# Performance work log

Hardware: AMD Instinct MI355X
Metric: run time of the kernel (lower is better)

The kernel has to match this reference:

```python
import jax, jax.numpy as jnp
import numpy as np

B, S, E, H, T, V = 32, 512, 256, 512, 8, 32000
G = 4 * H  # gate width


def setup_inputs() -> dict:
    key = jax.random.key(0)
    ks = jax.random.split(key, 14)
    s = 0.02  # init scale to keep tanh/sigmoid out of saturation
    return {
        "x": jax.random.randint(ks[0], (B, S), 0, V),
        "TASK": 0,
        "embed": jax.random.normal(ks[1], (V, E), jnp.float32) * s,
        "Wx_t": jax.random.normal(ks[2], (T, E, G), jnp.float32) * s,
        "Wh_t": jax.random.normal(ks[3], (T, H, G), jnp.float32) * s,
        "b_t": jnp.zeros((T, G), jnp.float32),
        "Ws_p1": jax.random.normal(ks[4], (H, H), jnp.float32) * s,
        "Ws_p2": jax.random.normal(ks[5], (H + E, H), jnp.float32) * s,
        "Us_w": jax.random.normal(ks[6], (H, 1), jnp.float32) * s,
        "Us_b": jnp.zeros((1,), jnp.float32),
        "Wx_c": jax.random.normal(ks[7], (E, G), jnp.float32) * s,
        "Wh_c": jax.random.normal(ks[8], (H, G), jnp.float32) * s,
        "Wm_c": jax.random.normal(ks[9], (H, G), jnp.float32) * s,
        "b_c": jnp.zeros((G,), jnp.float32),
    }


def _lstm_cell(g, c):
    i, f, gg, o = jnp.split(g, 4, axis=-1)
    c_new = jax.nn.sigmoid(f) * c + jax.nn.sigmoid(i) * jnp.tanh(gg)
    h_new = jax.nn.sigmoid(o) * jnp.tanh(c_new)
    return h_new, c_new


def _task_messages(emb, Wx, Wh, b):
    # emb [B,S,E]; Wx [K,E,4H]; returns aggregated messages [S,B,H,K]
    K = Wx.shape[0]
    xg = jnp.einsum('bse,keg->skbg', emb, Wx)  # precompute input gates [S,K,B,4H]
    h0 = jnp.zeros((K, emb.shape[0], Wh.shape[1]), emb.dtype)

    def step(carry, xg_t):
        h, c = carry  # [K,B,H]
        g = xg_t + jnp.einsum('kbh,khg->kbg', h, Wh) + b[:, None, :]
        h, c = _lstm_cell(g, c)
        return (h, c), h

    _, hs = jax.lax.scan(step, (h0, h0), xg)  # hs [S,K,B,H]
    return jnp.transpose(hs, (0, 2, 3, 1))  # [S,B,H,K]


def reference(x, TASK, embed, Wx_t, Wh_t, b_t, Ws_p1, Ws_p2, Us_w, Us_b,
              Wx_c, Wh_c, Wm_c, b_c):
    emb = embed[x]  # [B,S,E]
    other = np.array([i for i in range(Wx_t.shape[0]) if i != TASK])
    agg = _task_messages(emb, Wx_t[other], Wh_t[other], b_t[other])  # [S,B,H,K]

    emb_s = jnp.swapaxes(emb, 0, 1)          # [S,B,E]
    xg_c = emb_s @ Wx_c                       # [S,B,4H] precomputed input gates
    Bsz, Hdim = x.shape[0], Wh_c.shape[0]
    h0 = jnp.zeros((Bsz, Hdim), emb.dtype)

    def step(carry, inp):
        h, c = carry
        agg_t, emb_t, xg_t = inp  # [B,H,K], [B,E], [B,4H]
        # attention over the K task messages
        v1 = jnp.einsum('ij,bjk->bik', Ws_p1, agg_t) \
             + (jnp.concatenate([h, emb_t], axis=-1) @ Ws_p2)[:, :, None]
        v2 = jnp.tanh(v1)                                  # [B,H,K]
        Si = jnp.einsum('bhk,ho->bk', v2, Us_w) + Us_b     # [B,K]
        a = jax.nn.softmax(Si, axis=1)
        Rt = jnp.einsum('bk,bhk->bh', a, agg_t)            # [B,H]
        # custom LSTM cell step with message input Rt
        g = xg_t + h @ Wh_c + Rt @ Wm_c + b_c
        h, c = _lstm_cell(g, c)
        return (h, c), h

    (hN, cN), outs = jax.lax.scan(step, (h0, h0), (agg, emb_s, xg_c))
    out = jnp.swapaxes(outs, 0, 1)  # [B,S,H]
    return out, hN
```

## Files before the change

kernel.cpp:

```cpp
#include <hip/hip_runtime.h>

#define S_ 512
#define SCOPE __HIP_MEMORY_SCOPE_AGENT

typedef short bf16x8 __attribute__((ext_vector_type(8)));
typedef float f32x4 __attribute__((ext_vector_type(4)));

__device__ __forceinline__ float sigm(float x) { return 1.f / (1.f + expf(-x)); }
__device__ __forceinline__ float b2f(unsigned short u) {
    return __builtin_bit_cast(float, (unsigned)u << 16);
}
__device__ __forceinline__ unsigned short f2b(float f) {
    unsigned x = __builtin_bit_cast(unsigned, f);
    return (unsigned short)((x + 0x7fffu + ((x >> 16) & 1u)) >> 16);
}
__device__ __forceinline__ float ldcf(const float* p) {
    return __hip_atomic_load(p, __ATOMIC_RELAXED, SCOPE);
}
__device__ __forceinline__ unsigned ldc32(const void* p) {
    return __hip_atomic_load((const unsigned*)p, __ATOMIC_RELAXED, SCOPE);
}
__device__ __forceinline__ unsigned long long ldc64(const void* p) {
    return __hip_atomic_load((const unsigned long long*)p, __ATOMIC_RELAXED, SCOPE);
}
__device__ __forceinline__ void stg32(void* p, unsigned v) {
    __hip_atomic_store((unsigned*)p, v, __ATOMIC_RELAXED, SCOPE);
}
__device__ __forceinline__ void stgf(float* p, float v) {
    __hip_atomic_store(p, v, __ATOMIC_RELAXED, SCOPE);
}
__device__ __forceinline__ bf16x8 frag_c(const unsigned short* p) {
    union { unsigned long long q[2]; bf16x8 v; } u;
    u.q[0] = ldc64(p); u.q[1] = ldc64(p + 4);
    return u.v;
}
__device__ __forceinline__ bf16x8 frag_p(const unsigned short* p) {
    return *(const bf16x8*)p;
}
__device__ __forceinline__ void spin_ge(unsigned* p, unsigned thr) {
    while (__hip_atomic_load(p, __ATOMIC_RELAXED, SCOPE) < thr)
        __builtin_amdgcn_s_sleep(1);
}

__device__ __forceinline__ void gbar(unsigned* bar, int tid, int wg, unsigned n) {
    __syncthreads();
    if (tid == 0) {
        int g = wg >> 5;
        unsigned* gcnt = bar + 64 + g * 32;
        unsigned* ggen = bar + 320 + g * 32;
        unsigned old = __hip_atomic_fetch_add(gcnt, 1u, __ATOMIC_RELAXED, SCOPE);
        if (old == n * 32u - 1u) {
            unsigned rold = __hip_atomic_fetch_add(bar, 1u, __ATOMIC_RELAXED, SCOPE);
            if (rold == n * 8u - 1u) {
                __hip_atomic_store(bar + 32, n, __ATOMIC_RELAXED, SCOPE);
            } else {
                while (__hip_atomic_load(bar + 32, __ATOMIC_RELAXED, SCOPE) < n)
                    __builtin_amdgcn_s_sleep(1);
            }
            __hip_atomic_store(ggen, n, __ATOMIC_RELAXED, SCOPE);
        } else {
            while (__hip_atomic_load(ggen, __ATOMIC_RELAXED, SCOPE) < n)
                __builtin_amdgcn_s_sleep(1);
        }
        asm volatile("" ::: "memory");
    }
    __syncthreads();
}

__device__ __forceinline__ void gbar2(unsigned* bar, int tid, int wg, unsigned bn) {
    __syncthreads();
    if (tid == 0) stg32(bar + 1024 + wg * 32, bn);
    if (wg == 0) {
        if (tid < 256) spin_ge(bar + 1024 + tid * 32, bn);
        __syncthreads();
        if (tid == 0) stg32(bar + 576, bn);
    } else {
        if (tid == 0) spin_ge(bar + 576, bn);
        __syncthreads();
    }
}

__global__ __launch_bounds__(512) void fused_all(
        const int* __restrict__ x, const int* __restrict__ taskp,
        const float* __restrict__ embed,
        const float* __restrict__ Wx_t, const float* __restrict__ Wh_t,
        const float* __restrict__ b_t,
        const float* __restrict__ Ws_p1, const float* __restrict__ Ws_p2,
        const float* __restrict__ Us_w,
        const float* __restrict__ Wx_c, const float* __restrict__ Wh_c,
        const float* __restrict__ Wm_c, const float* __restrict__ b_c,
        float* __restrict__ out,
        unsigned short* __restrict__ WTa,  unsigned short* __restrict__ WTp2,
        unsigned short* __restrict__ WTp1, unsigned short* __restrict__ WTc,
        unsigned short* __restrict__ embbf, unsigned short* __restrict__ hbf,
        unsigned short* __restrict__ hmbf,
        float* __restrict__ ctask, float* __restrict__ cmain,
        float* __restrict__ p2w, float* __restrict__ partial,
        float* __restrict__ hNf, unsigned* __restrict__ bar)
{
    __shared__ float smem[8320];
    __shared__ unsigned short swA[64 * 776];
    const int wg = blockIdx.x, tid = threadIdx.x;
    const int lane = tid & 63, wave = tid >> 6;
    const int rowm = lane & 15, ks = lane >> 4;
    const int task = taskp[0];
    unsigned bn = 0;

    for (int i = wg * 512 + tid; i < 114688; i += 131072) stg32((unsigned*)hbf + i, 0u);
    for (int i = wg * 512 + tid; i < 16384; i += 131072) stg32((unsigned*)hmbf + i, 0u);
    for (int i = wg * 512 + tid; i < 114688; i += 131072) stgf(ctask + i, 0.f);
    for (int i = wg * 512 + tid; i < 16384; i += 131072) stgf(cmain + i, 0.f);
    for (int i = wg * 512 + tid; i < 2097152; i += 131072) {
        int ts = i >> 12, b = (i >> 7) & 31, ep = i & 127;
        int tok = x[b * S_ + ts];
        const float* s = embed + (size_t)tok * 256 + 2 * ep;
        stg32((unsigned*)embbf + i, (unsigned)f2b(s[0]) | ((unsigned)f2b(s[1]) << 16));
    }
    for (int i = wg * 512 + tid; i < 5505024; i += 131072) {
        int s = i / 24576, r = i % 24576, kp = r >> 6, cg = r & 63;
        int k = s >> 5, nt = s & 31, kk = k + (k >= task);
        int col = ((cg >> 4) << 9) + nt * 16 + (cg & 15);
        int kr = kp * 2;
        const float* src = (kr < 256)
            ? Wx_t + (size_t)kk * 524288 + (size_t)kr * 2048 + col
            : Wh_t + (size_t)kk * 1048576 + (size_t)(kr - 256) * 2048 + col;
        stg32((unsigned*)WTa + (size_t)s * 24576 + cg * 384 + kp,
              (unsigned)f2b(src[0]) | ((unsigned)f2b(src[2048]) << 16));
    }
    for (int i = wg * 512 + tid; i < 196608; i += 131072) {
        int p = i / 24576, r = i % 24576, kp = r >> 6, cg = r & 63;
        int col = p * 64 + cg, kr = kp * 2;
        const float* src = Ws_p2 + (size_t)kr * 512 + col;
        stg32((unsigned*)WTp2 + p * 24576 + cg * 384 + kp,
              (unsigned)f2b(src[0]) | ((unsigned)f2b(src[512]) << 16));
    }
    for (int i = wg * 512 + tid; i < 131072; i += 131072) {
        const float* src = Ws_p1 + 2 * (size_t)i;
        stg32((unsigned*)WTp1 + i, (unsigned)f2b(src[0]) | ((unsigned)f2b(src[1]) << 16));
    }
    for (int i = wg * 512 + tid; i < 1310720; i += 131072) {
        int ntc = i / 10240, r = i % 10240, kp = r >> 4, cg = r & 15;
        int col = ((cg >> 2) << 9) + ntc * 4 + (cg & 3);
        int kr = kp * 2;
        const float* src = (kr < 256) ? Wx_c + (size_t)kr * 2048 + col
                         : (kr < 768) ? Wh_c + (size_t)(kr - 256) * 2048 + col
                                      : Wm_c + (size_t)(kr - 768) * 2048 + col;
        stg32((unsigned*)WTc + ntc * 10240 + cg * 640 + kp,
              (unsigned)f2b(src[0]) | ((unsigned)f2b(src[2048]) << 16));
    }
    gbar(bar, tid, wg, 1);

    if (wg < 232) {
        const unsigned* srcw = (const unsigned*)(wg < 224
            ? WTa + (size_t)wg * 49152 : WTp2 + (size_t)(wg - 224) * 49152);
        for (int i = tid; i < 24576; i += 512) {
            int cg = i / 384, kp = i % 384;
            ((unsigned*)(swA + cg * 776))[kp] = srcw[cg * 384 + kp];
        }
    }
    __syncthreads();

    const int xq = wg & 7, jq = wg >> 3;
    const int kB = jq >> 2, itB = xq + 8 * (jq & 3);

    for (int t = 0; t < S_; ++t) {
        const int old = t & 1, nw = old ^ 1;
        const unsigned short* hb_old = hbf + old * 114688;
        unsigned short* hb_new = hbf + nw * 114688;
        const unsigned short* hm_old = hmbf + old * 16384;
        unsigned short* hm_new = hmbf + nw * 16384;
        const unsigned short* et = embbf + (size_t)t * 8192;

        if (wg < 232) {
            const bool istask = wg < 224;
            unsigned short* sh = (unsigned short*)smem;
            const unsigned short* hsrc = istask ? hb_old + (wg >> 5) * 16384 : hm_old;
            for (int i = tid; i < 4096; i += 512) {
                int row = i >> 7, c8 = i & 127;
                *(unsigned long long*)(sh + row * 520 + c8 * 4) =
                    ldc64(hsrc + row * 512 + c8 * 4);
            }
            __syncthreads();
            f32x4 acc = {0.f, 0.f, 0.f, 0.f};
            if (istask) {
                int k = wg >> 5, nt = wg & 31;
                int mt = wave >> 2, g = wave & 3;
                int b = mt * 16 + rowm;
                const unsigned short* wtp = swA + (g * 16 + rowm) * 776;
                const unsigned short* ep_ = et + b * 256;
                const unsigned short* shb = sh + b * 520;
#pragma unroll
                for (int kt = 0; kt < 24; ++kt) {
                    int ko = kt * 32 + ks * 8;
                    bf16x8 bf = frag_p(wtp + ko);
                    bf16x8 af = (kt < 8) ? frag_p(ep_ + ko) : frag_p(shb + ko - 256);
                    acc = __builtin_amdgcn_mfma_f32_16x16x32_bf16(af, bf, acc, 0, 0, 0);
                }
                __syncthreads();
                float* sg = smem;
#pragma unroll
                for (int r2 = 0; r2 < 4; ++r2)
                    sg[(mt * 16 + (lane >> 4) * 4 + r2) * 64 + g * 16 + rowm] = acc[r2];
                __syncthreads();
                {
                    int b2 = tid >> 4, hc = tid & 15;
                    int kk = k + (k >= task);
                    const float* bb = b_t + kk * 2048 + nt * 16 + hc;
                    float gi = sg[b2 * 64 + hc]      + bb[0];
                    float gf = sg[b2 * 64 + 16 + hc] + bb[512];
                    float gg = sg[b2 * 64 + 32 + hc] + bb[1024];
                    float go = sg[b2 * 64 + 48 + hc] + bb[1536];
                    int cidx = (k * 32 + b2) * 512 + nt * 16 + hc;
                    float cold = ctask[cidx];
                    float cn = sigm(gf) * cold + sigm(gi) * tanhf(gg);
                    float hn = sigm(go) * tanhf(cn);
                    ctask[cidx] = cn;
                    int hbits = (int)f2b(hn);
                    int oth = __shfl_xor(hbits, 1, 64);
                    if ((hc & 1) == 0)
                        stg32(hb_new + cidx, (unsigned)hbits | ((unsigned)oth << 16));
                }
            } else {
                int pb = wg - 224;
                int mt = wave >> 2, q = wave & 3;
                int b = mt * 16 + rowm;
                int cg = q * 16 + rowm;
                const unsigned short* wtp = swA + cg * 776;
                const unsigned short* ep_ = et + b * 256;
                const unsigned short* shb = sh + b * 520;
#pragma unroll
                for (int kt = 0; kt < 24; ++kt) {
                    int ko = kt * 32 + ks * 8;
                    bf16x8 bf = frag_p(wtp + ko);
                    bf16x8 af = (kt < 16) ? frag_p(shb + ko) : frag_p(ep_ + ko - 512);
                    acc = __builtin_amdgcn_mfma_f32_16x16x32_bf16(af, bf, acc, 0, 0, 0);
                }
#pragma unroll
                for (int r2 = 0; r2 < 4; ++r2)
                    stgf(p2w + (mt * 16 + (lane >> 4) * 4 + r2) * 512 + pb * 64 + cg, acc[r2]);
            }
        }
        gbar2(bar, tid, wg, ++bn);

        if (wg < 224) {
            int mt = wave & 1, kq = wave >> 1;
            f32x4 acc = {0.f, 0.f, 0.f, 0.f};
            const unsigned short* wtp = WTp1 + (itB * 16 + rowm) * 512;
            const unsigned short* hp_ = hb_new + (kB * 32 + mt * 16 + rowm) * 512;
#pragma unroll
            for (int s4 = 0; s4 < 4; ++s4) {
                int ko = (kq * 4 + s4) * 32 + ks * 8;
                bf16x8 bf = frag_p(wtp + ko);
                bf16x8 af = frag_c(hp_ + ko);
                acc = __builtin_amdgcn_mfma_f32_16x16x32_bf16(af, bf, acc, 0, 0, 0);
            }
            ((f32x4*)smem)[wave * 64 + lane] = acc;
            __syncthreads();
            {
                int b2 = tid >> 4, i2 = tid & 15;
                int mt2 = b2 >> 4, rr = b2 & 15;
                int ln = ((rr & 12) << 2) | i2, rg = rr & 3;
                float val = 0.f;
#pragma unroll
                for (int q2 = 0; q2 < 4; ++q2)
                    val += smem[((q2 * 2 + mt2) * 64 + ln) * 4 + rg];
                val += ldcf(p2w + b2 * 512 + itB * 16 + i2);
                float sv = tanhf(val) * Us_w[itB * 16 + i2];
                sv += __shfl_xor(sv, 1, 64); sv += __shfl_xor(sv, 2, 64);
                sv += __shfl_xor(sv, 4, 64); sv += __shfl_xor(sv, 8, 64);
                if (i2 == 0) stgf(partial + (kB * 32 + itB) * 32 + b2, sv);
            }
        }
        gbar2(bar, tid, wg, ++bn);

        {
            int mh = wg >> 7, ntc = wg & 127;
            unsigned short* Rt = (unsigned short*)smem;
            float* sredc = smem + 4160;
            float* ssi = smem + 6208;
            float* sa  = smem + 6320;
            float* sg2 = smem + 6432;
            float* sred4 = smem + 6688;
            if (tid < 448) {
                int kq = tid % 7, bl = (tid / 7) % 16, part = tid / 112;
                const float* pp = partial + (size_t)kq * 1024 + (size_t)(part * 8) * 32
                                + mh * 16 + bl;
                float v0 = ldcf(pp);        float v1 = ldcf(pp + 32);
                float v2 = ldcf(pp + 64);   float v3 = ldcf(pp + 96);
                float v4 = ldcf(pp + 128);  float v5 = ldcf(pp + 160);
                float v6 = ldcf(pp + 192);  float v7 = ldcf(pp + 224);
                sred4[part * 112 + bl * 7 + kq] =
                    ((v0 + v1) + (v2 + v3)) + ((v4 + v5) + (v6 + v7));
            }
            __syncthreads();
            if (tid < 112)
                ssi[tid] = (sred4[tid] + sred4[112 + tid])
                         + (sred4[224 + tid] + sred4[336 + tid]);
            __syncthreads();
            if (tid < 16) {
                float mx = -1e30f;
                for (int kq = 0; kq < 7; ++kq) mx = fmaxf(mx, ssi[tid * 7 + kq]);
                float den = 0.f, e[7];
                for (int kq = 0; kq < 7; ++kq) { e[kq] = expf(ssi[tid * 7 + kq] - mx); den += e[kq]; }
                float rd = 1.f / den;
                for (int kq = 0; kq < 7; ++kq) sa[tid * 7 + kq] = e[kq] * rd;
            }
            __syncthreads();
            for (int i = tid; i < 4096; i += 512) {
                int bl = i >> 8, rp = i & 255;
                const unsigned short* hb0 = hb_new + (mh * 16 + bl) * 512 + 2 * rp;
                unsigned u0 = ldc32(hb0);
                unsigned u1 = ldc32(hb0 + 16384);
                unsigned u2 = ldc32(hb0 + 32768);
                unsigned u3 = ldc32(hb0 + 49152);
                unsigned u4 = ldc32(hb0 + 65536);
                unsigned u5 = ldc32(hb0 + 81920);
                unsigned u6 = ldc32(hb0 + 98304);
                const float* sab = sa + bl * 7;
                float a0 = 0.f, a1 = 0.f;
                a0 = fmaf(sab[0], b2f((unsigned short)u0), a0);
                a1 = fmaf(sab[0], b2f((unsigned short)(u0 >> 16)), a1);
                a0 = fmaf(sab[1], b2f((unsigned short)u1), a0);
                a1 = fmaf(sab[1], b2f((unsigned short)(u1 >> 16)), a1);
                a0 = fmaf(sab[2], b2f((unsigned short)u2), a0);
                a1 = fmaf(sab[2], b2f((unsigned short)(u2 >> 16)), a1);
                a0 = fmaf(sab[3], b2f((unsigned short)u3), a0);
                a1 = fmaf(sab[3], b2f((unsigned short)(u3 >> 16)), a1);
                a0 = fmaf(sab[4], b2f((unsigned short)u4), a0);
                a1 = fmaf(sab[4], b2f((unsigned short)(u4 >> 16)), a1);
                a0 = fmaf(sab[5], b2f((unsigned short)u5), a0);
                a1 = fmaf(sab[5], b2f((unsigned short)(u5 >> 16)), a1);
                a0 = fmaf(sab[6], b2f((unsigned short)u6), a0);
                a1 = fmaf(sab[6], b2f((unsigned short)(u6 >> 16)), a1);
                Rt[bl * 520 + 2 * rp]     = f2b(a0);
                Rt[bl * 520 + 2 * rp + 1] = f2b(a1);
            }
            __syncthreads();
            f32x4 acc = {0.f, 0.f, 0.f, 0.f};
            const unsigned short* wtp = WTc + (size_t)ntc * 20480 + rowm * 1280;
            int b = mh * 16 + rowm;
            const unsigned short* ep_ = et + b * 256;
            const unsigned short* hp_ = hm_old + b * 512;
            const unsigned short* rp_ = Rt + rowm * 520;
#pragma unroll
            for (int s5 = 0; s5 < 5; ++s5) {
                int kt = wave * 5 + s5;
                int ko = kt * 32 + ks * 8;
                bf16x8 bf = frag_p(wtp + ko);
                bf16x8 af;
                if (kt < 8) af = frag_p(ep_ + ko);
                else if (kt < 24) af = frag_c(hp_ + ko - 256);
                else af = frag_p(rp_ + ko - 768);
                acc = __builtin_amdgcn_mfma_f32_16x16x32_bf16(af, bf, acc, 0, 0, 0);
            }
            __syncthreads();
            ((f32x4*)sredc)[wave * 64 + lane] = acc;
            __syncthreads();
            if (tid < 256) {
                int rr = tid >> 4, c = tid & 15;
                int ln = ((rr & 12) << 2) | c, rg = rr & 3;
                float val = 0.f;
#pragma unroll
                for (int w2 = 0; w2 < 8; ++w2) val += sredc[(w2 * 64 + ln) * 4 + rg];
                sg2[rr * 16 + c] = val;
            }
            __syncthreads();
            if (tid < 64) {
                int bl = tid >> 2, j = tid & 3;
                int b2 = mh * 16 + bl;
                int colh = ntc * 4 + j;
                float gi = sg2[bl * 16 + 0  + j] + b_c[colh];
                float gf = sg2[bl * 16 + 4  + j] + b_c[512 + colh];
                float gg = sg2[bl * 16 + 8  + j] + b_c[1024 + colh];
                float go = sg2[bl * 16 + 12 + j] + b_c[1536 + colh];
                int cidx = b2 * 512 + colh;
                float cold = cmain[cidx];
                float cn = sigm(gf) * cold + sigm(gi) * tanhf(gg);
                float hn = sigm(go) * tanhf(cn);
                cmain[cidx] = cn;
                out[(size_t)b2 * 262144 + (size_t)t * 512 + colh] = hn;
                int hbits = (int)f2b(hn);
                int oth = __shfl_xor(hbits, 1, 64);
                if ((j & 1) == 0)
                    stg32(hm_new + cidx, (unsigned)hbits | ((unsigned)oth << 16));
                if (t == 511) stgf(hNf + cidx, hn);
            }
        }
        gbar2(bar, tid, wg, ++bn);
    }

    for (int i = wg * 512 + tid; i < 16384; i += 131072)
        out[8388608 + i] = ldcf(hNf + i);
}

extern "C" void kernel_launch(void* const* d_in, const int* in_sizes, int n_in,
                              void* d_out, int out_size, void* d_ws, size_t ws_size,
                              hipStream_t stream) {
    const int*   x      = (const int*)d_in[0];
    const int*   taskp  = (const int*)d_in[1];
    const float* embed  = (const float*)d_in[2];
    const float* Wx_t   = (const float*)d_in[3];
    const float* Wh_t   = (const float*)d_in[4];
    const float* b_t    = (const float*)d_in[5];
    const float* Ws_p1  = (const float*)d_in[6];
    const float* Ws_p2  = (const float*)d_in[7];
    const float* Us_w   = (const float*)d_in[8];
    const float* Wx_c   = (const float*)d_in[10];
    const float* Wh_c   = (const float*)d_in[11];
    const float* Wm_c   = (const float*)d_in[12];
    const float* b_c    = (const float*)d_in[13];
    float* out = (float*)d_out;

    unsigned short* us = (unsigned short*)d_ws;
    unsigned short* WTa   = us;
    unsigned short* WTp2  = WTa   + 11010048;
    unsigned short* WTp1  = WTp2  + 393216;
    unsigned short* WTc   = WTp1  + 262144;
    unsigned short* embbf = WTc   + 2621440;
    unsigned short* hbf   = embbf + 4194304;
    unsigned short* hmbf  = hbf   + 229376;
    float* fb      = (float*)(hmbf + 32768);
    float* ctask   = fb;
    float* cmain   = ctask + 114688;
    float* p2w     = cmain + 16384;
    float* partial = p2w   + 16384;
    float* hNf     = partial + 7168;
    unsigned* bar  = (unsigned*)(hNf + 16384);

    hipMemsetAsync(bar, 0, 40960, stream);

    void* args[] = { (void*)&x, (void*)&taskp, (void*)&embed,
                     (void*)&Wx_t, (void*)&Wh_t, (void*)&b_t,
                     (void*)&Ws_p1, (void*)&Ws_p2, (void*)&Us_w,
                     (void*)&Wx_c, (void*)&Wh_c, (void*)&Wm_c, (void*)&b_c,
                     (void*)&out,
                     (void*)&WTa, (void*)&WTp2, (void*)&WTp1, (void*)&WTc,
                     (void*)&embbf, (void*)&hbf, (void*)&hmbf,
                     (void*)&ctask, (void*)&cmain, (void*)&p2w, (void*)&partial,
                     (void*)&hNf, (void*)&bar };
    hipLaunchCooperativeKernel((void*)fused_all, dim3(256), dim3(512), args, 0, stream);
}
```

Baseline: 9.752 ms.

## Relax end-of-step barrier for task blocks and prefetch embeddings and messages early

The grid barrier is rewritten so the master block becomes the last block, and at the end of each timestep only attention/projection blocks (wg>=224) wait for release. Task-LSTM blocks proceed straight into the next step's work, since they only depend on their own previous h. Embedding fragments are preloaded into registers before the shared-memory barrier. The seven task message vectors are issued as loads before the softmax reduction so their latency overlaps it. This adds register pressure and a final spin on the barrier counter before hN is copied out, and it relies on task blocks not overrunning data still being read by other blocks.

```diff
diff --git a/kernel.cpp b/kernel.cpp
--- a/kernel.cpp
+++ b/kernel.cpp
@@ -67,14 +67,15 @@
     __syncthreads();
 }
 
-__device__ __forceinline__ void gbar2(unsigned* bar, int tid, int wg, unsigned bn) {
+__device__ __forceinline__ void gbar3(unsigned* bar, int tid, int wg, unsigned bn,
+                                      bool wait) {
     __syncthreads();
     if (tid == 0) stg32(bar + 1024 + wg * 32, bn);
-    if (wg == 0) {
+    if (wg == 255) {
         if (tid < 256) spin_ge(bar + 1024 + tid * 32, bn);
         __syncthreads();
         if (tid == 0) stg32(bar + 576, bn);
-    } else {
+    } else if (wait) {
         if (tid == 0) spin_ge(bar + 576, bn);
         __syncthreads();
     }
@@ -98,7 +99,7 @@
         float* __restrict__ p2w, float* __restrict__ partial,
         float* __restrict__ hNf, unsigned* __restrict__ bar)
 {
-    __shared__ float smem[8320];
+    __shared__ float smem[9344];
     __shared__ unsigned short swA[64 * 776];
     const int wg = blockIdx.x, tid = threadIdx.x;
     const int lane = tid & 63, wave = tid >> 6;
@@ -175,25 +176,29 @@
             const bool istask = wg < 224;
             unsigned short* sh = (unsigned short*)smem;
             const unsigned short* hsrc = istask ? hb_old + (wg >> 5) * 16384 : hm_old;
+            const int mt = wave >> 2, g = wave & 3;
+            const int bA = mt * 16 + rowm;
+            const unsigned short* ep_ = et + bA * 256;
             for (int i = tid; i < 4096; i += 512) {
                 int row = i >> 7, c8 = i & 127;
                 *(unsigned long long*)(sh + row * 520 + c8 * 4) =
                     ldc64(hsrc + row * 512 + c8 * 4);
             }
+            bf16x8 ee[8];
+#pragma unroll
+            for (int j = 0; j < 8; ++j) ee[j] = frag_p(ep_ + j * 32 + ks * 8);
             __syncthreads();
             f32x4 acc = {0.f, 0.f, 0.f, 0.f};
             if (istask) {
                 int k = wg >> 5, nt = wg & 31;
-                int mt = wave >> 2, g = wave & 3;
-                int b = mt * 16 + rowm;
                 const unsigned short* wtp = swA + (g * 16 + rowm) * 776;
-                const unsigned short* ep_ = et + b * 256;
-                const unsigned short* shb = sh + b * 520;
+                const unsigned short* shb = sh + bA * 520;
 #pragma unroll
                 for (int kt = 0; kt < 24; ++kt) {
                     int ko = kt * 32 + ks * 8;
                     bf16x8 bf = frag_p(wtp + ko);
-                    bf16x8 af = (kt < 8) ? frag_p(ep_ + ko) : frag_p(shb + ko - 256);
+                    bf16x8 af = (kt < 8) ? ee[kt < 8 ? kt : 0]
+                                         : frag_p(shb + ko - 256);
                     acc = __builtin_amdgcn_mfma_f32_16x16x32_bf16(af, bf, acc, 0, 0, 0);
                 }
                 __syncthreads();
@@ -222,17 +227,15 @@
                 }
             } else {
                 int pb = wg - 224;
-                int mt = wave >> 2, q = wave & 3;
-                int b = mt * 16 + rowm;
-                int cg = q * 16 + rowm;
+                int cg = g * 16 + rowm;
                 const unsigned short* wtp = swA + cg * 776;
-                const unsigned short* ep_ = et + b * 256;
-                const unsigned short* shb = sh + b * 520;
+                const unsigned short* shb = sh + bA * 520;
 #pragma unroll
                 for (int kt = 0; kt < 24; ++kt) {
                     int ko = kt * 32 + ks * 8;
                     bf16x8 bf = frag_p(wtp + ko);
-                    bf16x8 af = (kt < 16) ? frag_p(shb + ko) : frag_p(ep_ + ko - 512);
+                    bf16x8 af = (kt < 16) ? frag_p(shb + ko)
+                                          : ee[kt >= 16 ? kt - 16 : 0];
                     acc = __builtin_amdgcn_mfma_f32_16x16x32_bf16(af, bf, acc, 0, 0, 0);
                 }
 #pragma unroll
@@ -240,7 +243,7 @@
                     stgf(p2w + (mt * 16 + (lane >> 4) * 4 + r2) * 512 + pb * 64 + cg, acc[r2]);
             }
         }
-        gbar2(bar, tid, wg, ++bn);
+        gbar3(bar, tid, wg, ++bn, true);
 
         if (wg < 224) {
             int mt = wave & 1, kq = wave >> 1;
@@ -271,16 +274,26 @@
                 if (i2 == 0) stgf(partial + (kB * 32 + itB) * 32 + b2, sv);
             }
         }
-        gbar2(bar, tid, wg, ++bn);
+        gbar3(bar, tid, wg, ++bn, true);
 
         {
             int mh = wg >> 7, ntc = wg & 127;
-            unsigned short* Rt = (unsigned short*)smem;
-            float* sredc = smem + 4160;
-            float* ssi = smem + 6208;
-            float* sa  = smem + 6320;
-            float* sg2 = smem + 6432;
-            float* sred4 = smem + 6688;
+            unsigned short* Rt = (unsigned short*)(smem + 4160);
+            float* sredc = smem;
+            float* ssi = smem + 8320;
+            float* sa  = smem + 8432;
+            float* sg2 = smem + 8544;
+            float* sred4 = smem + 8800;
+            unsigned uu[8][7];
+#pragma unroll
+            for (int j = 0; j < 8; ++j) {
+                int i = tid + 512 * j;
+                int bl = i >> 8, rp = i & 255;
+                const unsigned short* hb0 = hb_new + (mh * 16 + bl) * 512 + 2 * rp;
+#pragma unroll
+                for (int kq = 0; kq < 7; ++kq)
+                    uu[j][kq] = ldc32(hb0 + kq * 16384);
+            }
             if (tid < 448) {
                 int kq = tid % 7, bl = (tid / 7) % 16, part = tid / 112;
                 const float* pp = partial + (size_t)kq * 1024 + (size_t)(part * 8) * 32
@@ -306,32 +319,18 @@
                 for (int kq = 0; kq < 7; ++kq) sa[tid * 7 + kq] = e[kq] * rd;
             }
             __syncthreads();
-            for (int i = tid; i < 4096; i += 512) {
+#pragma unroll
+            for (int j = 0; j < 8; ++j) {
+                int i = tid + 512 * j;
                 int bl = i >> 8, rp = i & 255;
-                const unsigned short* hb0 = hb_new + (mh * 16 + bl) * 512 + 2 * rp;
-                unsigned u0 = ldc32(hb0);
-                unsigned u1 = ldc32(hb0 + 16384);
-                unsigned u2 = ldc32(hb0 + 32768);
-                unsigned u3 = ldc32(hb0 + 49152);
-                unsigned u4 = ldc32(hb0 + 65536);
-                unsigned u5 = ldc32(hb0 + 81920);
-                unsigned u6 = ldc32(hb0 + 98304);
                 const float* sab = sa + bl * 7;
                 float a0 = 0.f, a1 = 0.f;
-                a0 = fmaf(sab[0], b2f((unsigned short)u0), a0);
-                a1 = fmaf(sab[0], b2f((unsigned short)(u0 >> 16)), a1);
-                a0 = fmaf(sab[1], b2f((unsigned short)u1), a0);
-                a1 = fmaf(sab[1], b2f((unsigned short)(u1 >> 16)), a1);
-                a0 = fmaf(sab[2], b2f((unsigned short)u2), a0);
-                a1 = fmaf(sab[2], b2f((unsigned short)(u2 >> 16)), a1);
-                a0 = fmaf(sab[3], b2f((unsigned short)u3), a0);
-                a1 = fmaf(sab[3], b2f((unsigned short)(u3 >> 16)), a1);
-                a0 = fmaf(sab[4], b2f((unsigned short)u4), a0);
-                a1 = fmaf(sab[4], b2f((unsigned short)(u4 >> 16)), a1);
-                a0 = fmaf(sab[5], b2f((unsigned short)u5), a0);
-                a1 = fmaf(sab[5], b2f((unsigned short)(u5 >> 16)), a1);
-                a0 = fmaf(sab[6], b2f((unsigned short)u6), a0);
-                a1 = fmaf(sab[6], b2f((unsigned short)(u6 >> 16)), a1);
+#pragma unroll
+                for (int kq = 0; kq < 7; ++kq) {
+                    unsigned u = uu[j][kq];
+                    a0 = fmaf(sab[kq], b2f((unsigned short)u), a0);
+                    a1 = fmaf(sab[kq], b2f((unsigned short)(u >> 16)), a1);
+                }
                 Rt[bl * 520 + 2 * rp]     = f2b(a0);
                 Rt[bl * 520 + 2 * rp + 1] = f2b(a1);
             }
@@ -386,9 +385,11 @@
                 if (t == 511) stgf(hNf + cidx, hn);
             }
         }
-        gbar2(bar, tid, wg, ++bn);
-    }
-
+        gbar3(bar, tid, wg, ++bn, wg >= 224);
+    }
+
+    if (tid == 0) spin_ge(bar + 576, 1536u);
+    __syncthreads();
     for (int i = wg * 512 + tid; i < 16384; i += 131072)
         out[8388608 + i] = ldcf(hNf + i);
 }
```

Result: faster. 9.449 ms (-3.1%).
